# Performance work log

Hardware: AMD Instinct MI355X
Metric: run time of the kernel (lower is better)

## Reference

```python
import jax, jax.numpy as jnp
import numpy as np

N_NODES = 50000
N_EDGES = 800000
IN_CH = 128
HID = 64
NUM_HEADS = 8
NUM_CLASSES = 2
NEG_SLOPE = 0.2   # PyG GATConv default LeakyReLU slope
BN_EPS = 1e-5
SOFTMAX_EPS = 1e-16  # PyG softmax denominator epsilon


def setup_inputs() -> dict:
    key = jax.random.key(0)
    ks = jax.random.split(key, 20)
    s = 0.1
    inp = {
        "x": jax.random.normal(ks[0], (N_NODES, IN_CH), dtype=jnp.float32),
        "edge_index": jax.random.randint(ks[1], (2, N_EDGES), 0, N_NODES, dtype=jnp.int64),
        # layer 0 params, stacked over the 8 independent heads
        "W0": jax.random.normal(ks[2], (NUM_HEADS, IN_CH, HID), dtype=jnp.float32) * s,
        "a_src0": jax.random.normal(ks[3], (NUM_HEADS, HID), dtype=jnp.float32) * s,
        "a_dst0": jax.random.normal(ks[4], (NUM_HEADS, HID), dtype=jnp.float32) * s,
        "b0": jnp.zeros((NUM_HEADS, HID), dtype=jnp.float32),
        "gamma0": jnp.ones((NUM_HEADS, HID), dtype=jnp.float32),
        "beta0": jnp.zeros((NUM_HEADS, HID), dtype=jnp.float32),
        # layer 1 params
        "W1": jax.random.normal(ks[5], (NUM_HEADS, HID, HID), dtype=jnp.float32) * s,
        "a_src1": jax.random.normal(ks[6], (NUM_HEADS, HID), dtype=jnp.float32) * s,
        "a_dst1": jax.random.normal(ks[7], (NUM_HEADS, HID), dtype=jnp.float32) * s,
        "b1": jnp.zeros((NUM_HEADS, HID), dtype=jnp.float32),
        "gamma1": jnp.ones((NUM_HEADS, HID), dtype=jnp.float32),
        "beta1": jnp.zeros((NUM_HEADS, HID), dtype=jnp.float32),
        # ensemble classifier
        "Wc": jax.random.normal(ks[8], (NUM_HEADS * HID, NUM_CLASSES), dtype=jnp.float32) * s,
        "bc": jnp.zeros((NUM_CLASSES,), dtype=jnp.float32),
    }
    return inp


def _gat_layer(x, src, dst, n, W, a_s, a_d, b):
    """Single-head GATConv (PyG semantics, self-loops already in src/dst)."""
    h = x @ W                                           # [N, C]
    logits = (h @ a_s)[src] + (h @ a_d)[dst]            # [E]
    logits = jax.nn.leaky_relu(logits, NEG_SLOPE)
    m = jax.ops.segment_max(logits, dst, num_segments=n)
    ex = jnp.exp(logits - m[dst])
    denom = jax.ops.segment_sum(ex, dst, num_segments=n)
    alpha = ex / (denom[dst] + SOFTMAX_EPS)             # segment softmax over dst
    out = jax.ops.segment_sum(h[src] * alpha[:, None], dst, num_segments=n)
    return out + b


def _bn(h, gamma, beta):
    # BatchNorm1d training-mode math (batch statistics over nodes)
    mu = jnp.mean(h, axis=0)
    var = jnp.var(h, axis=0)
    return (h - mu) * jax.lax.rsqrt(var + BN_EPS) * gamma + beta


def reference(x, edge_index, W0, a_src0, a_dst0, b0, gamma0, beta0,
              W1, a_src1, a_dst1, b1, gamma1, beta1, Wc, bc):
    n = x.shape[0]
    loops = jnp.arange(n, dtype=edge_index.dtype)
    src = jnp.concatenate([edge_index[0], loops])  # PyG add_self_loops=True
    dst = jnp.concatenate([edge_index[1], loops])

    def branch(Wh0, as0, ad0, bh0, g0, be0, Wh1, as1, ad1, bh1, g1, be1):
        h = _gat_layer(x, src, dst, n, Wh0, as0, ad0, bh0)
        h = jax.nn.elu(_bn(h, g0, be0))                  # dropout off (eval)
        h = _gat_layer(h, src, dst, n, Wh1, as1, ad1, bh1)
        h = jax.nn.elu(_bn(h, g1, be1))
        return h                                          # [N, HID]

    hs = jax.vmap(branch)(W0, a_src0, a_dst0, b0, gamma0, beta0,
                          W1, a_src1, a_dst1, b1, gamma1, beta1)  # [H, N, HID]
    feat = jnp.transpose(hs, (1, 0, 2)).reshape(n, -1)            # [N, H*HID]
    return feat @ Wc + bc
```

## Files before the change

### kernel.cpp

```cpp
#include <hip/hip_runtime.h>
#include <hip/hip_bf16.h>
#include <math.h>
#include <stdint.h>

#define N_NODES 50000
#define N_EDGES 800000
#define E_TOT   (N_EDGES + N_NODES)
#define IN_CH   128
#define HID     64
#define NHEAD   8
#define C       512
#define NEG_SLOPE 0.2f
#define BN_EPS    1e-5f
#define SM_EPS    1e-16f
#define SCAN_B    196
#define STAT_B    256

typedef __attribute__((ext_vector_type(8))) short bf16x8;
typedef __attribute__((ext_vector_type(4))) float f32x4;

__device__ __forceinline__ float lrelu(float x){ return x > 0.f ? x : NEG_SLOPE * x; }
__device__ __forceinline__ float elu(float x){ return x > 0.f ? x : __expf(x) - 1.f; }
__device__ __forceinline__ float bflo(unsigned u){ return __uint_as_float(u << 16); }
__device__ __forceinline__ float bfhi(unsigned u){ return __uint_as_float(u & 0xffff0000u); }
__device__ __forceinline__ float bfu(unsigned short u){ return __uint_as_float(((unsigned)u) << 16); }
__device__ __forceinline__ unsigned short f2bf(float f){
  unsigned u = __float_as_uint(f);
  unsigned r = u + 0x7fffu + ((u >> 16) & 1u);
  return (unsigned short)(r >> 16);
}

__global__ void k_detect(const int* __restrict__ ei, int* flag){
  if (threadIdx.x == 0 && blockIdx.x == 0) {
    int f = 1;
    for (int i = 0; i < 32; i++) if (ei[2*i + 1] != 0) f = 0;
    *flag = f;
  }
}
__global__ void k_init_counts(int* counts){
  int i = blockIdx.x * 256 + threadIdx.x;
  if (i < N_NODES) counts[i] = 1;
}
__global__ void k_extract_count(const int* __restrict__ ei, const int* __restrict__ flag,
                                int* __restrict__ src32, int* __restrict__ dst32,
                                int* counts){
  int e = blockIdx.x * 256 + threadIdx.x;
  if (e >= N_EDGES) return;
  int s, d;
  if (*flag) {
    const long long* e64 = (const long long*)ei;
    s = (int)e64[e];
    d = (int)e64[(size_t)N_EDGES + e];
  } else {
    s = ei[e];
    d = ei[N_EDGES + e];
  }
  src32[e] = s; dst32[e] = d;
  atomicAdd(&counts[d], 1);
}

__global__ void k_scan1(const int* __restrict__ counts, int* __restrict__ excl, int* __restrict__ bsum){
  __shared__ int s[256];
  int tid = threadIdx.x;
  int i = blockIdx.x * 256 + tid;
  int v = (i < N_NODES) ? counts[i] : 0;
  s[tid] = v; __syncthreads();
#pragma unroll
  for (int d = 1; d < 256; d <<= 1) {
    int t = (tid >= d) ? s[tid - d] : 0;
    __syncthreads(); s[tid] += t; __syncthreads();
  }
  if (i < N_NODES) excl[i] = s[tid] - v;
  if (tid == 255) bsum[blockIdx.x] = s[255];
}
__global__ void k_scan2(int* bsum){
  __shared__ int s[256];
  int tid = threadIdx.x;
  int v = (tid < SCAN_B) ? bsum[tid] : 0;
  s[tid] = v; __syncthreads();
#pragma unroll
  for (int d = 1; d < 256; d <<= 1) {
    int t = (tid >= d) ? s[tid - d] : 0;
    __syncthreads(); s[tid] += t; __syncthreads();
  }
  if (tid < SCAN_B) bsum[tid] = s[tid] - v;
}
__global__ void k_scan3(const int* __restrict__ excl, const int* __restrict__ bsum,
                        int* __restrict__ off, int* __restrict__ cursor, int* __restrict__ csr){
  int i = blockIdx.x * 256 + threadIdx.x;
  if (i < N_NODES) {
    int o = excl[i] + bsum[blockIdx.x];
    off[i] = o; cursor[i] = o + 1; csr[o] = i;
  }
  if (i == 0) off[N_NODES] = E_TOT;
}
__global__ void k_scatter_edges(const int* __restrict__ src, const int* __restrict__ dst,
                                int* cursor, int* __restrict__ csr_src){
  int e = blockIdx.x * 256 + threadIdx.x;
  if (e < N_EDGES) { int d = dst[e]; int p = atomicAdd(&cursor[d], 1); csr_src[p] = src[e]; }
}

__global__ void k_cast_x(const float* __restrict__ X, unsigned short* __restrict__ X16){
  size_t i = (size_t)(blockIdx.x * 256 + threadIdx.x) * 4;
  float4 v = *reinterpret_cast<const float4*>(&X[i]);
  ushort4 p; p.x = f2bf(v.x); p.y = f2bf(v.y); p.z = f2bf(v.z); p.w = f2bf(v.w);
  *reinterpret_cast<ushort4*>(&X16[i]) = p;
}
template<int K>
__global__ void k_transpose_w(const float* __restrict__ W, unsigned short* __restrict__ Bt){
  int i = blockIdx.x * 256 + threadIdx.x;
  int k = i % K; int rem = i / K; int c = rem & 63; int h = rem >> 6;
  Bt[i] = f2bf(W[((size_t)h * K + k) * 64 + c]);
}

__global__ __launch_bounds__(256) void k_gemm0(const unsigned short* __restrict__ X16,
                                               const unsigned short* __restrict__ Bt,
                                               const float* __restrict__ a_src,
                                               const float* __restrict__ a_dst,
                                               unsigned short* __restrict__ H16,
                                               float* __restrict__ s_src,
                                               float* __restrict__ s_dst){
  __shared__ unsigned short LA[64 * 136];
  __shared__ unsigned short LB[64 * 136];
  int r0 = blockIdx.x * 64, h = blockIdx.y;
  int tid = threadIdx.x;
#pragma unroll
  for (int i = 0; i < 4; i++) {
    int idx = tid + i * 256;
    int r = idx >> 4, l16 = idx & 15;
    uint4 v = make_uint4(0, 0, 0, 0);
    if (r0 + r < N_NODES)
      v = *reinterpret_cast<const uint4*>(&X16[(size_t)(r0 + r) * IN_CH + l16 * 8]);
    *reinterpret_cast<uint4*>(&LA[r * 136 + l16 * 8]) = v;
  }
#pragma unroll
  for (int i = 0; i < 4; i++) {
    int idx = tid + i * 256;
    int c = idx >> 4, l16 = idx & 15;
    uint4 v = *reinterpret_cast<const uint4*>(&Bt[(size_t)h * 8192 + c * 128 + l16 * 8]);
    *reinterpret_cast<uint4*>(&LB[c * 136 + l16 * 8]) = v;
  }
  __syncthreads();
  int w = tid >> 6, l = tid & 63;
  int lr = l & 15, lg = l >> 4;
  f32x4 acc[4] = {};
#pragma unroll
  for (int kf = 0; kf < 4; kf++) {
    bf16x8 af = *reinterpret_cast<const bf16x8*>(&LA[(w * 16 + lr) * 136 + kf * 32 + lg * 8]);
#pragma unroll
    for (int cf = 0; cf < 4; cf++) {
      bf16x8 bfr = *reinterpret_cast<const bf16x8*>(&LB[(cf * 16 + lr) * 136 + kf * 32 + lg * 8]);
      acc[cf] = __builtin_amdgcn_mfma_f32_16x16x32_bf16(af, bfr, acc[cf], 0, 0, 0);
    }
  }
#pragma unroll
  for (int cf = 0; cf < 4; cf++)
#pragma unroll
    for (int rr = 0; rr < 4; rr++) {
      int gr = r0 + w * 16 + lg * 4 + rr;
      if (gr < N_NODES)
        H16[(size_t)gr * C + h * HID + cf * 16 + lr] = f2bf(acc[cf][rr]);
    }
  float ps[4] = {}, pd[4] = {};
#pragma unroll
  for (int cf = 0; cf < 4; cf++) {
    float as_ = a_src[h * HID + cf * 16 + lr];
    float ad_ = a_dst[h * HID + cf * 16 + lr];
#pragma unroll
    for (int rr = 0; rr < 4; rr++) { ps[rr] += acc[cf][rr] * as_; pd[rr] += acc[cf][rr] * ad_; }
  }
#pragma unroll
  for (int rr = 0; rr < 4; rr++)
#pragma unroll
    for (int o = 1; o < 16; o <<= 1) { ps[rr] += __shfl_xor(ps[rr], o, 64); pd[rr] += __shfl_xor(pd[rr], o, 64); }
  if (lr == 0) {
#pragma unroll
    for (int rr = 0; rr < 4; rr++) {
      int gr = r0 + w * 16 + lg * 4 + rr;
      if (gr < N_NODES) { s_src[gr * NHEAD + h] = ps[rr]; s_dst[gr * NHEAD + h] = pd[rr]; }
    }
  }
}

__global__ __launch_bounds__(256) void k_gemm1(const unsigned short* __restrict__ Hb,
                                               const unsigned short* __restrict__ Bt,
                                               const float* __restrict__ scale,
                                               const float* __restrict__ shift,
                                               const float* __restrict__ a_src,
                                               const float* __restrict__ a_dst,
                                               unsigned short* __restrict__ H16,
                                               float* __restrict__ s_src,
                                               float* __restrict__ s_dst){
  __shared__ unsigned short LA[64 * 72];
  __shared__ unsigned short LB[64 * 72];
  int r0 = blockIdx.x * 64, h = blockIdx.y;
  int tid = threadIdx.x;
#pragma unroll
  for (int i = 0; i < 4; i++) {
    int idx = tid + i * 256;
    int r = idx >> 4, l16 = idx & 15;
    ushort4 hv = make_ushort4(0, 0, 0, 0);
    if (r0 + r < N_NODES)
      hv = *reinterpret_cast<const ushort4*>(&Hb[(size_t)(r0 + r) * C + h * HID + l16 * 4]);
    float4 sc = *reinterpret_cast<const float4*>(&scale[h * HID + l16 * 4]);
    float4 sh = *reinterpret_cast<const float4*>(&shift[h * HID + l16 * 4]);
    ushort4 p;
    p.x = f2bf(elu(sc.x * bfu(hv.x) + sh.x));
    p.y = f2bf(elu(sc.y * bfu(hv.y) + sh.y));
    p.z = f2bf(elu(sc.z * bfu(hv.z) + sh.z));
    p.w = f2bf(elu(sc.w * bfu(hv.w) + sh.w));
    *reinterpret_cast<ushort4*>(&LA[r * 72 + l16 * 4]) = p;
  }
#pragma unroll
  for (int i = 0; i < 2; i++) {
    int idx = tid + i * 256;
    int c = idx >> 3, l8 = idx & 7;
    uint4 v = *reinterpret_cast<const uint4*>(&Bt[(size_t)h * 4096 + c * 64 + l8 * 8]);
    *reinterpret_cast<uint4*>(&LB[c * 72 + l8 * 8]) = v;
  }
  __syncthreads();
  int w = tid >> 6, l = tid & 63;
  int lr = l & 15, lg = l >> 4;
  f32x4 acc[4] = {};
#pragma unroll
  for (int kf = 0; kf < 2; kf++) {
    bf16x8 af = *reinterpret_cast<const bf16x8*>(&LA[(w * 16 + lr) * 72 + kf * 32 + lg * 8]);
#pragma unroll
    for (int cf = 0; cf < 4; cf++) {
      bf16x8 bfr = *reinterpret_cast<const bf16x8*>(&LB[(cf * 16 + lr) * 72 + kf * 32 + lg * 8]);
      acc[cf] = __builtin_amdgcn_mfma_f32_16x16x32_bf16(af, bfr, acc[cf], 0, 0, 0);
    }
  }
#pragma unroll
  for (int cf = 0; cf < 4; cf++)
#pragma unroll
    for (int rr = 0; rr < 4; rr++) {
      int gr = r0 + w * 16 + lg * 4 + rr;
      if (gr < N_NODES)
        H16[(size_t)gr * C + h * HID + cf * 16 + lr] = f2bf(acc[cf][rr]);
    }
  float ps[4] = {}, pd[4] = {};
#pragma unroll
  for (int cf = 0; cf < 4; cf++) {
    float as_ = a_src[h * HID + cf * 16 + lr];
    float ad_ = a_dst[h * HID + cf * 16 + lr];
#pragma unroll
    for (int rr = 0; rr < 4; rr++) { ps[rr] += acc[cf][rr] * as_; pd[rr] += acc[cf][rr] * ad_; }
  }
#pragma unroll
  for (int rr = 0; rr < 4; rr++)
#pragma unroll
    for (int o = 1; o < 16; o <<= 1) { ps[rr] += __shfl_xor(ps[rr], o, 64); pd[rr] += __shfl_xor(pd[rr], o, 64); }
  if (lr == 0) {
#pragma unroll
    for (int rr = 0; rr < 4; rr++) {
      int gr = r0 + w * 16 + lg * 4 + rr;
      if (gr < N_NODES) { s_src[gr * NHEAD + h] = ps[rr]; s_dst[gr * NHEAD + h] = pd[rr]; }
    }
  }
}

__global__ __launch_bounds__(256) void k_aggregate(const unsigned short* __restrict__ H16,
                                                   const float* __restrict__ s_src,
                                                   const float* __restrict__ s_dst,
                                                   const int* __restrict__ off,
                                                   const int* __restrict__ csr,
                                                   const float* __restrict__ bias,
                                                   unsigned short* __restrict__ HoutB){
  __shared__ float alds[4][64][8];
  int wv = threadIdx.x >> 6, lane = threadIdx.x & 63;
  int n = blockIdx.x * 4 + wv;
  if (n >= N_NODES) return;
  int e0 = off[n], deg = off[n + 1] - e0;
  int hsel = lane >> 3;

  float sd[NHEAD];
#pragma unroll
  for (int h = 0; h < NHEAD; h++) sd[h] = s_dst[n * NHEAD + h];

  float acc[8] = {};
  float dnl[NHEAD] = {};

  for (int base = 0; base < deg; base += 64) {
    int e = base + lane;
    int cnt = min(64, deg - base);
    int s_reg = 0;
    if (e < deg) {
      s_reg = csr[e0 + e];
      const float4* sp = reinterpret_cast<const float4*>(&s_src[s_reg * NHEAD]);
      float4 s01 = sp[0], s23 = sp[1];
      float sv[8] = { s01.x, s01.y, s01.z, s01.w, s23.x, s23.y, s23.z, s23.w };
#pragma unroll
      for (int h = 0; h < NHEAD; h++) {
        float ex = __expf(lrelu(sv[h] + sd[h]));
        dnl[h] += ex;
        alds[wv][lane][h] = ex;
      }
    }
#pragma unroll 2
    for (int j = 0; j < cnt; j++) {
      int s = __shfl(s_reg, j, 64);
      float a = alds[wv][j][hsel];
      const uint4* rp = reinterpret_cast<const uint4*>(H16 + (size_t)s * C);
      uint4 v = rp[lane];
      acc[0] += a * bflo(v.x); acc[1] += a * bfhi(v.x);
      acc[2] += a * bflo(v.y); acc[3] += a * bfhi(v.y);
      acc[4] += a * bflo(v.z); acc[5] += a * bfhi(v.z);
      acc[6] += a * bflo(v.w); acc[7] += a * bfhi(v.w);
    }
  }

  float mydn = 0.f;
#pragma unroll
  for (int h = 0; h < NHEAD; h++) {
    float d = dnl[h];
#pragma unroll
    for (int o = 32; o; o >>= 1) d += __shfl_xor(d, o, 64);
    if (hsel == h) mydn = d;
  }
  float inv = 1.f / (mydn + SM_EPS);

  const float* bp = bias + lane * 8;
  ushort4 p0, p1;
  p0.x = f2bf(acc[0]*inv + bp[0]); p0.y = f2bf(acc[1]*inv + bp[1]);
  p0.z = f2bf(acc[2]*inv + bp[2]); p0.w = f2bf(acc[3]*inv + bp[3]);
  p1.x = f2bf(acc[4]*inv + bp[4]); p1.y = f2bf(acc[5]*inv + bp[5]);
  p1.z = f2bf(acc[6]*inv + bp[6]); p1.w = f2bf(acc[7]*inv + bp[7]);
  unsigned short* op = HoutB + (size_t)n * C + lane * 8;
  *reinterpret_cast<ushort4*>(op) = p0;
  *reinterpret_cast<ushort4*>(op + 4) = p1;
}

__global__ __launch_bounds__(256) void k_bn_stats(const unsigned short* __restrict__ Hb,
                                                  float* __restrict__ partial){
  __shared__ float red[4][64][16];
  int tid = threadIdx.x, w = tid >> 6, c64 = tid & 63;
  float s[8] = {}, q[8] = {};
  for (int r = blockIdx.x * 4 + w; r < N_NODES; r += gridDim.x * 4) {
    uint4 v = *reinterpret_cast<const uint4*>(&Hb[(size_t)r * C + c64 * 8]);
    float f[8] = { bflo(v.x), bfhi(v.x), bflo(v.y), bfhi(v.y),
                   bflo(v.z), bfhi(v.z), bflo(v.w), bfhi(v.w) };
#pragma unroll
    for (int k = 0; k < 8; k++) { s[k] += f[k]; q[k] += f[k] * f[k]; }
  }
#pragma unroll
  for (int k = 0; k < 8; k++) { red[w][c64][k] = s[k]; red[w][c64][k + 8] = q[k]; }
  __syncthreads();
  if (w == 0) {
#pragma unroll
    for (int k = 0; k < 8; k++) {
      float ss = red[0][c64][k] + red[1][c64][k] + red[2][c64][k] + red[3][c64][k];
      float qq = red[0][c64][k+8] + red[1][c64][k+8] + red[2][c64][k+8] + red[3][c64][k+8];
      partial[(size_t)blockIdx.x * 1024 + c64 * 8 + k] = ss;
      partial[(size_t)blockIdx.x * 1024 + 512 + c64 * 8 + k] = qq;
    }
  }
}
__global__ void k_bn_finalize(const float* __restrict__ partial, const float* __restrict__ gamma,
                              const float* __restrict__ beta, float* __restrict__ scale,
                              float* __restrict__ shift){
  int c = threadIdx.x;
  float s = 0.f, q = 0.f;
  for (int b = 0; b < STAT_B; b++) {
    s += partial[(size_t)b * 1024 + c];
    q += partial[(size_t)b * 1024 + 512 + c];
  }
  float mean = s * (1.f / N_NODES);
  float var  = q * (1.f / N_NODES) - mean * mean;
  float sc = gamma[c] * rsqrtf(var + BN_EPS);
  scale[c] = sc;
  shift[c] = beta[c] - mean * sc;
}

__global__ __launch_bounds__(256) void k_final(const unsigned short* __restrict__ Hb,
                                               const float* __restrict__ scale,
                                               const float* __restrict__ shift,
                                               const float* __restrict__ Wc,
                                               const float* __restrict__ bc,
                                               float* __restrict__ out){
  int wave = threadIdx.x >> 6, lane = threadIdx.x & 63;
  int n = blockIdx.x * 4 + wave;
  if (n >= N_NODES) return;
  uint4 v = *reinterpret_cast<const uint4*>(&Hb[(size_t)n * C + lane * 8]);
  float f[8] = { bflo(v.x), bfhi(v.x), bflo(v.y), bfhi(v.y),
                 bflo(v.z), bfhi(v.z), bflo(v.w), bfhi(v.w) };
  float4 sc0 = *reinterpret_cast<const float4*>(&scale[lane * 8]);
  float4 sc1 = *reinterpret_cast<const float4*>(&scale[lane * 8 + 4]);
  float4 sh0 = *reinterpret_cast<const float4*>(&shift[lane * 8]);
  float4 sh1 = *reinterpret_cast<const float4*>(&shift[lane * 8 + 4]);
  float scv[8] = { sc0.x, sc0.y, sc0.z, sc0.w, sc1.x, sc1.y, sc1.z, sc1.w };
  float shv[8] = { sh0.x, sh0.y, sh0.z, sh0.w, sh1.x, sh1.y, sh1.z, sh1.w };
  float a0 = 0.f, a1 = 0.f;
#pragma unroll
  for (int k = 0; k < 8; k++) {
    float t = elu(scv[k] * f[k] + shv[k]);
    int ch = lane * 8 + k;
    a0 += t * Wc[ch * 2 + 0];
    a1 += t * Wc[ch * 2 + 1];
  }
#pragma unroll
  for (int o = 32; o; o >>= 1) { a0 += __shfl_xor(a0, o, 64); a1 += __shfl_xor(a1, o, 64); }
  if (lane == 0) { out[n * 2 + 0] = a0 + bc[0]; out[n * 2 + 1] = a1 + bc[1]; }
}

extern "C" void kernel_launch(void* const* d_in, const int* in_sizes, int n_in,
                              void* d_out, int out_size, void* d_ws, size_t ws_size,
                              hipStream_t stream) {
  const float* x      = (const float*)d_in[0];
  const int*   ei     = (const int*)d_in[1];
  const float* W0     = (const float*)d_in[2];
  const float* a_src0 = (const float*)d_in[3];
  const float* a_dst0 = (const float*)d_in[4];
  const float* b0     = (const float*)d_in[5];
  const float* gamma0 = (const float*)d_in[6];
  const float* beta0  = (const float*)d_in[7];
  const float* W1     = (const float*)d_in[8];
  const float* a_src1 = (const float*)d_in[9];
  const float* a_dst1 = (const float*)d_in[10];
  const float* b1     = (const float*)d_in[11];
  const float* gamma1 = (const float*)d_in[12];
  const float* beta1  = (const float*)d_in[13];
  const float* Wc     = (const float*)d_in[14];
  const float* bc     = (const float*)d_in[15];
  float* out = (float*)d_out;

  char* ws = (char*)d_ws;
  size_t o = 0;
  auto alloc = [&](size_t bytes) { char* p = ws + o; o = (o + bytes + 255) & ~(size_t)255; return p; };
  int*   flag    = (int*)  alloc(4);
  int*   src32   = (int*)  alloc((size_t)N_EDGES * 4);
  int*   dst32   = (int*)  alloc((size_t)N_EDGES * 4);
  int*   counts  = (int*)  alloc((size_t)N_NODES * 4);
  int*   excl    = (int*)  alloc((size_t)N_NODES * 4);
  int*   bsum    = (int*)  alloc(256 * 4);
  int*   off     = (int*)  alloc((size_t)(N_NODES + 1) * 4);
  int*   cursor  = (int*)  alloc((size_t)N_NODES * 4);
  int*   csr     = (int*)  alloc((size_t)E_TOT * 4);
  float* s_src   = (float*)alloc((size_t)N_NODES * NHEAD * 4);
  float* s_dst   = (float*)alloc((size_t)N_NODES * NHEAD * 4);
  float* partial = (float*)alloc((size_t)STAT_B * 1024 * 4);
  float* scale   = (float*)alloc(C * 4);
  float* shift   = (float*)alloc(C * 4);
  unsigned short* x16  = (unsigned short*)alloc((size_t)N_NODES * IN_CH * 2);
  unsigned short* bt0  = (unsigned short*)alloc((size_t)NHEAD * HID * IN_CH * 2);
  unsigned short* bt1  = (unsigned short*)alloc((size_t)NHEAD * HID * HID * 2);
  unsigned short* h16a = (unsigned short*)alloc((size_t)N_NODES * C * 2);
  unsigned short* h16b = (unsigned short*)alloc((size_t)N_NODES * C * 2);

  const int GE = (N_EDGES + 255) / 256;
  const int GN = (N_NODES + 255) / 256;
  const int GW = (N_NODES + 3) / 4;
  const int GR = (N_NODES + 63) / 64;

  k_detect<<<1, 64, 0, stream>>>(ei, flag);
  k_init_counts<<<GN, 256, 0, stream>>>(counts);
  k_extract_count<<<GE, 256, 0, stream>>>(ei, flag, src32, dst32, counts);

  k_cast_x<<<(N_NODES * IN_CH / 4 + 255) / 256, 256, 0, stream>>>(x, x16);
  k_transpose_w<IN_CH><<<(NHEAD * HID * IN_CH + 255) / 256, 256, 0, stream>>>(W0, bt0);
  k_transpose_w<HID><<<(NHEAD * HID * HID + 255) / 256, 256, 0, stream>>>(W1, bt1);

  k_scan1<<<GN, 256, 0, stream>>>(counts, excl, bsum);
  k_scan2<<<1, 256, 0, stream>>>(bsum);
  k_scan3<<<GN, 256, 0, stream>>>(excl, bsum, off, cursor, csr);
  k_scatter_edges<<<GE, 256, 0, stream>>>(src32, dst32, cursor, csr);

  k_gemm0<<<dim3(GR, NHEAD), 256, 0, stream>>>(x16, bt0, a_src0, a_dst0, h16a, s_src, s_dst);
  k_aggregate<<<GW, 256, 0, stream>>>(h16a, s_src, s_dst, off, csr, b0, h16b);
  k_bn_stats<<<STAT_B, 256, 0, stream>>>(h16b, partial);
  k_bn_finalize<<<1, 512, 0, stream>>>(partial, gamma0, beta0, scale, shift);

  k_gemm1<<<dim3(GR, NHEAD), 256, 0, stream>>>(h16b, bt1, scale, shift, a_src1, a_dst1, h16a, s_src, s_dst);
  k_aggregate<<<GW, 256, 0, stream>>>(h16a, s_src, s_dst, off, csr, b1, h16b);
  k_bn_stats<<<STAT_B, 256, 0, stream>>>(h16b, partial);
  k_bn_finalize<<<1, 512, 0, stream>>>(partial, gamma1, beta1, scale, shift);

  k_final<<<GW, 256, 0, stream>>>(h16b, scale, shift, Wc, bc, out);
}
```

Before: 512.7 us.

## Fuse x cast into gemm0, loop heads in-block, batch aggregate gathers

Removes the separate fp32-to-bf16 cast kernel for x by converting inside gemm0 while staging the tile into LDS. gemm0 now loops over all 8 heads per row tile, so x is read once rather than eight times, at the cost of a grid eight times smaller and extra barriers. The aggregate kernel stores source indices in LDS and unrolls the gather loop by four, keeping several independent row loads in flight to hide memory latency.

After: 506.1 us. No clear change (-1.3%).

```diff
diff --git a/kernel.cpp b/kernel.cpp
--- a/kernel.cpp
+++ b/kernel.cpp
@@ -100,12 +100,6 @@
   if (e < N_EDGES) { int d = dst[e]; int p = atomicAdd(&cursor[d], 1); csr_src[p] = src[e]; }
 }
 
-__global__ void k_cast_x(const float* __restrict__ X, unsigned short* __restrict__ X16){
-  size_t i = (size_t)(blockIdx.x * 256 + threadIdx.x) * 4;
-  float4 v = *reinterpret_cast<const float4*>(&X[i]);
-  ushort4 p; p.x = f2bf(v.x); p.y = f2bf(v.y); p.z = f2bf(v.z); p.w = f2bf(v.w);
-  *reinterpret_cast<ushort4*>(&X16[i]) = p;
-}
 template<int K>
 __global__ void k_transpose_w(const float* __restrict__ W, unsigned short* __restrict__ Bt){
   int i = blockIdx.x * 256 + threadIdx.x;
@@ -113,7 +107,7 @@
   Bt[i] = f2bf(W[((size_t)h * K + k) * 64 + c]);
 }
 
-__global__ __launch_bounds__(256) void k_gemm0(const unsigned short* __restrict__ X16,
+__global__ __launch_bounds__(256) void k_gemm0(const float* __restrict__ X,
                                                const unsigned short* __restrict__ Bt,
                                                const float* __restrict__ a_src,
                                                const float* __restrict__ a_dst,
@@ -122,62 +116,72 @@
                                                float* __restrict__ s_dst){
   __shared__ unsigned short LA[64 * 136];
   __shared__ unsigned short LB[64 * 136];
-  int r0 = blockIdx.x * 64, h = blockIdx.y;
+  int r0 = blockIdx.x * 64;
   int tid = threadIdx.x;
 #pragma unroll
   for (int i = 0; i < 4; i++) {
     int idx = tid + i * 256;
     int r = idx >> 4, l16 = idx & 15;
-    uint4 v = make_uint4(0, 0, 0, 0);
-    if (r0 + r < N_NODES)
-      v = *reinterpret_cast<const uint4*>(&X16[(size_t)(r0 + r) * IN_CH + l16 * 8]);
-    *reinterpret_cast<uint4*>(&LA[r * 136 + l16 * 8]) = v;
-  }
-#pragma unroll
-  for (int i = 0; i < 4; i++) {
-    int idx = tid + i * 256;
-    int c = idx >> 4, l16 = idx & 15;
-    uint4 v = *reinterpret_cast<const uint4*>(&Bt[(size_t)h * 8192 + c * 128 + l16 * 8]);
-    *reinterpret_cast<uint4*>(&LB[c * 136 + l16 * 8]) = v;
-  }
-  __syncthreads();
+    float4 u0 = make_float4(0.f,0.f,0.f,0.f), u1 = u0;
+    if (r0 + r < N_NODES) {
+      const float* xp = &X[(size_t)(r0 + r) * IN_CH + l16 * 8];
+      u0 = *reinterpret_cast<const float4*>(xp);
+      u1 = *reinterpret_cast<const float4*>(xp + 4);
+    }
+    ushort4 p0, p1;
+    p0.x = f2bf(u0.x); p0.y = f2bf(u0.y); p0.z = f2bf(u0.z); p0.w = f2bf(u0.w);
+    p1.x = f2bf(u1.x); p1.y = f2bf(u1.y); p1.z = f2bf(u1.z); p1.w = f2bf(u1.w);
+    *reinterpret_cast<ushort4*>(&LA[r * 136 + l16 * 8]) = p0;
+    *reinterpret_cast<ushort4*>(&LA[r * 136 + l16 * 8 + 4]) = p1;
+  }
   int w = tid >> 6, l = tid & 63;
   int lr = l & 15, lg = l >> 4;
-  f32x4 acc[4] = {};
-#pragma unroll
-  for (int kf = 0; kf < 4; kf++) {
-    bf16x8 af = *reinterpret_cast<const bf16x8*>(&LA[(w * 16 + lr) * 136 + kf * 32 + lg * 8]);
+  for (int h = 0; h < NHEAD; h++) {
+    __syncthreads();
+#pragma unroll
+    for (int i = 0; i < 4; i++) {
+      int idx = tid + i * 256;
+      int c = idx >> 4, l16 = idx & 15;
+      uint4 v = *reinterpret_cast<const uint4*>(&Bt[(size_t)h * 8192 + c * 128 + l16 * 8]);
+      *reinterpret_cast<uint4*>(&LB[c * 136 + l16 * 8]) = v;
+    }
+    __syncthreads();
+    f32x4 acc[4] = {};
+#pragma unroll
+    for (int kf = 0; kf < 4; kf++) {
+      bf16x8 af = *reinterpret_cast<const bf16x8*>(&LA[(w * 16 + lr) * 136 + kf * 32 + lg * 8]);
+#pragma unroll
+      for (int cf = 0; cf < 4; cf++) {
+        bf16x8 bfr = *reinterpret_cast<const bf16x8*>(&LB[(cf * 16 + lr) * 136 + kf * 32 + lg * 8]);
+        acc[cf] = __builtin_amdgcn_mfma_f32_16x16x32_bf16(af, bfr, acc[cf], 0, 0, 0);
+      }
+    }
+#pragma unroll
+    for (int cf = 0; cf < 4; cf++)
+#pragma unroll
+      for (int rr = 0; rr < 4; rr++) {
+        int gr = r0 + w * 16 + lg * 4 + rr;
+        if (gr < N_NODES)
+          H16[(size_t)gr * C + h * HID + cf * 16 + lr] = f2bf(acc[cf][rr]);
+      }
+    float ps[4] = {}, pd[4] = {};
 #pragma unroll
     for (int cf = 0; cf < 4; cf++) {
-      bf16x8 bfr = *reinterpret_cast<const bf16x8*>(&LB[(cf * 16 + lr) * 136 + kf * 32 + lg * 8]);
-      acc[cf] = __builtin_amdgcn_mfma_f32_16x16x32_bf16(af, bfr, acc[cf], 0, 0, 0);
-    }
-  }
-#pragma unroll
-  for (int cf = 0; cf < 4; cf++)
-#pragma unroll
-    for (int rr = 0; rr < 4; rr++) {
-      int gr = r0 + w * 16 + lg * 4 + rr;
-      if (gr < N_NODES)
-        H16[(size_t)gr * C + h * HID + cf * 16 + lr] = f2bf(acc[cf][rr]);
-    }
-  float ps[4] = {}, pd[4] = {};
-#pragma unroll
-  for (int cf = 0; cf < 4; cf++) {
-    float as_ = a_src[h * HID + cf * 16 + lr];
-    float ad_ = a_dst[h * HID + cf * 16 + lr];
-#pragma unroll
-    for (int rr = 0; rr < 4; rr++) { ps[rr] += acc[cf][rr] * as_; pd[rr] += acc[cf][rr] * ad_; }
-  }
-#pragma unroll
-  for (int rr = 0; rr < 4; rr++)
-#pragma unroll
-    for (int o = 1; o < 16; o <<= 1) { ps[rr] += __shfl_xor(ps[rr], o, 64); pd[rr] += __shfl_xor(pd[rr], o, 64); }
-  if (lr == 0) {
-#pragma unroll
-    for (int rr = 0; rr < 4; rr++) {
-      int gr = r0 + w * 16 + lg * 4 + rr;
-      if (gr < N_NODES) { s_src[gr * NHEAD + h] = ps[rr]; s_dst[gr * NHEAD + h] = pd[rr]; }
+      float as_ = a_src[h * HID + cf * 16 + lr];
+      float ad_ = a_dst[h * HID + cf * 16 + lr];
+#pragma unroll
+      for (int rr = 0; rr < 4; rr++) { ps[rr] += acc[cf][rr] * as_; pd[rr] += acc[cf][rr] * ad_; }
+    }
+#pragma unroll
+    for (int rr = 0; rr < 4; rr++)
+#pragma unroll
+      for (int o = 1; o < 16; o <<= 1) { ps[rr] += __shfl_xor(ps[rr], o, 64); pd[rr] += __shfl_xor(pd[rr], o, 64); }
+    if (lr == 0) {
+#pragma unroll
+      for (int rr = 0; rr < 4; rr++) {
+        int gr = r0 + w * 16 + lg * 4 + rr;
+        if (gr < N_NODES) { s_src[gr * NHEAD + h] = ps[rr]; s_dst[gr * NHEAD + h] = pd[rr]; }
+      }
     }
   }
 }
@@ -267,7 +271,8 @@
                                                    const int* __restrict__ csr,
                                                    const float* __restrict__ bias,
                                                    unsigned short* __restrict__ HoutB){
-  __shared__ float alds[4][64][8];
+  __shared__ float aexp[4][64][8];
+  __shared__ int   sidx[4][64];
   int wv = threadIdx.x >> 6, lane = threadIdx.x & 63;
   int n = blockIdx.x * 4 + wv;
   if (n >= N_NODES) return;
@@ -284,25 +289,49 @@
   for (int base = 0; base < deg; base += 64) {
     int e = base + lane;
     int cnt = min(64, deg - base);
-    int s_reg = 0;
     if (e < deg) {
-      s_reg = csr[e0 + e];
-      const float4* sp = reinterpret_cast<const float4*>(&s_src[s_reg * NHEAD]);
+      int s = csr[e0 + e];
+      sidx[wv][lane] = s;
+      const float4* sp = reinterpret_cast<const float4*>(&s_src[s * NHEAD]);
       float4 s01 = sp[0], s23 = sp[1];
       float sv[8] = { s01.x, s01.y, s01.z, s01.w, s23.x, s23.y, s23.z, s23.w };
 #pragma unroll
       for (int h = 0; h < NHEAD; h++) {
         float ex = __expf(lrelu(sv[h] + sd[h]));
         dnl[h] += ex;
-        alds[wv][lane][h] = ex;
+        aexp[wv][lane][h] = ex;
       }
     }
-#pragma unroll 2
-    for (int j = 0; j < cnt; j++) {
-      int s = __shfl(s_reg, j, 64);
-      float a = alds[wv][j][hsel];
-      const uint4* rp = reinterpret_cast<const uint4*>(H16 + (size_t)s * C);
-      uint4 v = rp[lane];
+    int j = 0;
+    for (; j + 4 <= cnt; j += 4) {
+      int s0 = sidx[wv][j+0], s1 = sidx[wv][j+1], s2 = sidx[wv][j+2], s3 = sidx[wv][j+3];
+      float a0 = aexp[wv][j+0][hsel], a1 = aexp[wv][j+1][hsel];
+      float a2 = aexp[wv][j+2][hsel], a3 = aexp[wv][j+3][hsel];
+      uint4 v0 = reinterpret_cast<const uint4*>(H16 + (size_t)s0 * C)[lane];
+      uint4 v1 = reinterpret_cast<const uint4*>(H16 + (size_t)s1 * C)[lane];
+      uint4 v2 = reinterpret_cast<const uint4*>(H16 + (size_t)s2 * C)[lane];
+      uint4 v3 = reinterpret_cast<const uint4*>(H16 + (size_t)s3 * C)[lane];
+      acc[0] += a0 * bflo(v0.x); acc[1] += a0 * bfhi(v0.x);
+      acc[2] += a0 * bflo(v0.y); acc[3] += a0 * bfhi(v0.y);
+      acc[4] += a0 * bflo(v0.z); acc[5] += a0 * bfhi(v0.z);
+      acc[6] += a0 * bflo(v0.w); acc[7] += a0 * bfhi(v0.w);
+      acc[0] += a1 * bflo(v1.x); acc[1] += a1 * bfhi(v1.x);
+      acc[2] += a1 * bflo(v1.y); acc[3] += a1 * bfhi(v1.y);
+      acc[4] += a1 * bflo(v1.z); acc[5] += a1 * bfhi(v1.z);
+      acc[6] += a1 * bflo(v1.w); acc[7] += a1 * bfhi(v1.w);
+      acc[0] += a2 * bflo(v2.x); acc[1] += a2 * bfhi(v2.x);
+      acc[2] += a2 * bflo(v2.y); acc[3] += a2 * bfhi(v2.y);
+      acc[4] += a2 * bflo(v2.z); acc[5] += a2 * bfhi(v2.z);
+      acc[6] += a2 * bflo(v2.w); acc[7] += a2 * bfhi(v2.w);
+      acc[0] += a3 * bflo(v3.x); acc[1] += a3 * bfhi(v3.x);
+      acc[2] += a3 * bflo(v3.y); acc[3] += a3 * bfhi(v3.y);
+      acc[4] += a3 * bflo(v3.z); acc[5] += a3 * bfhi(v3.z);
+      acc[6] += a3 * bflo(v3.w); acc[7] += a3 * bfhi(v3.w);
+    }
+    for (; j < cnt; j++) {
+      int s = sidx[wv][j];
+      float a = aexp[wv][j][hsel];
+      uint4 v = reinterpret_cast<const uint4*>(H16 + (size_t)s * C)[lane];
       acc[0] += a * bflo(v.x); acc[1] += a * bfhi(v.x);
       acc[2] += a * bflo(v.y); acc[3] += a * bfhi(v.y);
       acc[4] += a * bflo(v.z); acc[5] += a * bfhi(v.z);
@@ -441,7 +470,6 @@
   float* partial = (float*)alloc((size_t)STAT_B * 1024 * 4);
   float* scale   = (float*)alloc(C * 4);
   float* shift   = (float*)alloc(C * 4);
-  unsigned short* x16  = (unsigned short*)alloc((size_t)N_NODES * IN_CH * 2);
   unsigned short* bt0  = (unsigned short*)alloc((size_t)NHEAD * HID * IN_CH * 2);
   unsigned short* bt1  = (unsigned short*)alloc((size_t)NHEAD * HID * HID * 2);
   unsigned short* h16a = (unsigned short*)alloc((size_t)N_NODES * C * 2);
@@ -456,7 +484,6 @@
   k_init_counts<<<GN, 256, 0, stream>>>(counts);
   k_extract_count<<<GE, 256, 0, stream>>>(ei, flag, src32, dst32, counts);
 
-  k_cast_x<<<(N_NODES * IN_CH / 4 + 255) / 256, 256, 0, stream>>>(x, x16);
   k_transpose_w<IN_CH><<<(NHEAD * HID * IN_CH + 255) / 256, 256, 0, stream>>>(W0, bt0);
   k_transpose_w<HID><<<(NHEAD * HID * HID + 255) / 256, 256, 0, stream>>>(W1, bt1);
 
@@ -465,7 +492,7 @@
   k_scan3<<<GN, 256, 0, stream>>>(excl, bsum, off, cursor, csr);
   k_scatter_edges<<<GE, 256, 0, stream>>>(src32, dst32, cursor, csr);
 
-  k_gemm0<<<dim3(GR, NHEAD), 256, 0, stream>>>(x16, bt0, a_src0, a_dst0, h16a, s_src, s_dst);
+  k_gemm0<<<GR, 256, 0, stream>>>(x, bt0, a_src0, a_dst0, h16a, s_src, s_dst);
   k_aggregate<<<GW, 256, 0, stream>>>(h16a, s_src, s_dst, off, csr, b0, h16b);
   k_bn_stats<<<STAT_B, 256, 0, stream>>>(h16b, partial);
   k_bn_finalize<<<1, 512, 0, stream>>>(partial, gamma0, beta0, scale, shift);
```
